# Performance work log

Measured on AMD Instinct MI355X. Metric: run time of the kernel, lower is better.

The kernel has to match this reference:

```python
import jax, jax.numpy as jnp
import numpy as np

CAPACITY = 0.125


def setup_inputs() -> dict:
    key = jax.random.key(0)
    ks = jax.random.split(key, 6)
    b, s, d, dff = 4, 8192, 512, 2048
    x = jax.random.normal(ks[0], (b, s, d), dtype=jnp.float32)
    position_ids = jnp.tile(jnp.arange(s, dtype=jnp.int64)[None, :], (b, 1))
    Wr = jax.random.normal(ks[1], (d,), dtype=jnp.float32) * 0.02
    br = jnp.zeros((1,), dtype=jnp.float32)
    W1 = jax.random.normal(ks[2], (d, dff), dtype=jnp.float32) * 0.02
    b1 = jnp.zeros((dff,), dtype=jnp.float32)
    W2 = jax.random.normal(ks[3], (dff, d), dtype=jnp.float32) * 0.02
    b2 = jnp.zeros((d,), dtype=jnp.float32)
    return {"x": x, "position_ids": position_ids, "Wr": Wr, "br": br,
            "W1": W1, "b1": b1, "W2": W2, "b2": b2}


def reference(x, position_ids, Wr, br, W1, b1, W2, b2):
    b, s, d = x.shape
    # Router: Linear(d, 1) -> squeeze(-1)
    weights = jnp.einsum('bsd,d->bs', x, Wr) + br  # [b, s]
    k = int(CAPACITY * s)
    # Per-batch top-k threshold (k-th largest value)
    top_k_values = jax.lax.top_k(weights, k)[0]  # [b, k], sorted desc
    threshold = top_k_values[:, -1]              # [b]
    selected_mask = weights > threshold[:, None]  # strict >, ties excluded (matches torch)
    # Block: per-token MLP (Linear-GELU-Linear). Per-token ops commute with the
    # gather/scatter, so computing densely and masking is mathematically identical
    # to the original gather -> block -> weighted scatter.
    h = jax.nn.gelu(jnp.einsum('bsd,df->bsf', x, W1) + b1)
    y = jnp.einsum('bsf,fd->bsd', h, W2) + b2
    # processed_tokens (= block_out * router_weight on selected) + x on unselected
    out = jnp.where(selected_mask[..., None], y * weights[..., None], x)
    return out
```

## Files before the change

### kernel.cpp

```cpp
#include <hip/hip_runtime.h>
#include <hip/hip_bf16.h>

#define B_   4
#define S_   8192
#define D_   512
#define DFF_ 2048
#define K_TOP 1024

typedef unsigned short u16;
typedef __attribute__((ext_vector_type(8))) short bf16x8;
typedef __attribute__((ext_vector_type(4))) float floatx4;

__device__ __forceinline__ unsigned f2key(float f){
    unsigned u = __float_as_uint(f);
    return (u & 0x80000000u) ? ~u : (u | 0x80000000u);
}
__device__ __forceinline__ u16 f2b(float f){
    unsigned u = __float_as_uint(f);
    u = (u + 0x7FFFu + ((u >> 16) & 1u)) >> 16;
    return (u16)u;
}
__device__ __forceinline__ float gelu_tanh(float v){
    float c = 0.7978845608028654f * (v + 0.044715f * v * v * v);
    return 0.5f * v * (1.0f + tanhf(c));
}

__global__ __launch_bounds__(256) void wts_copy_kernel(
    const float4* __restrict__ x, float4* __restrict__ out,
    const float4* __restrict__ Wr4, const float* __restrict__ br,
    float* __restrict__ w_all, int* __restrict__ count)
{
    if (blockIdx.x == 0 && threadIdx.x == 0) *count = 0;
    const int wv = threadIdx.x >> 6, lane = threadIdx.x & 63;
    const int token = blockIdx.x * 4 + wv;
    const float4* xt = x + (size_t)token * 128;
    float acc = 0.f;
    #pragma unroll
    for (int i = 0; i < 2; i++){
        int j = lane + i * 64;
        float4 v = xt[j];
        out[(size_t)token * 128 + j] = v;
        float4 wvv = Wr4[j];
        acc += v.x*wvv.x + v.y*wvv.y + v.z*wvv.z + v.w*wvv.w;
    }
    #pragma unroll
    for (int off = 32; off > 0; off >>= 1) acc += __shfl_down(acc, off, 64);
    if (lane == 0) w_all[token] = acc + br[0];
}

__global__ __launch_bounds__(1024) void kth_compact_kernel(
    const float4* __restrict__ w_all4, int* __restrict__ count,
    int* __restrict__ idx)
{
    __shared__ unsigned keys[S_];
    __shared__ unsigned hist[16][256];
    __shared__ unsigned suffix[256];
    __shared__ unsigned sprefix;
    __shared__ int sremk;
    const int b = blockIdx.x, tid = threadIdx.x, wv = tid >> 6;
    const float4* row4 = w_all4 + (size_t)b * (S_ / 4);

    #pragma unroll
    for (int i = 0; i < 2; i++){
        int j = tid + i * 1024;
        float4 v = row4[j];
        keys[4*j+0] = f2key(v.x); keys[4*j+1] = f2key(v.y);
        keys[4*j+2] = f2key(v.z); keys[4*j+3] = f2key(v.w);
    }
    if (tid == 0){ sprefix = 0u; sremk = K_TOP; }
    __syncthreads();

    for (int pass = 3; pass >= 0; pass--){
        for (int i = tid; i < 16 * 256; i += 1024) ((unsigned*)hist)[i] = 0u;
        __syncthreads();
        const unsigned mask_hi = (pass == 3) ? 0u : (0xFFFFFFFFu << ((pass + 1) * 8));
        const unsigned pfx = sprefix;
        const int shift = pass * 8;
        #pragma unroll
        for (int i = 0; i < 8; i++){
            unsigned key = keys[tid + i * 1024];
            if ((key & mask_hi) == pfx)
                atomicAdd(&hist[wv][(key >> shift) & 255u], 1u);
        }
        __syncthreads();
        if (tid < 256){
            unsigned s = 0;
            #pragma unroll
            for (int h = 0; h < 16; h++) s += hist[h][tid];
            suffix[tid] = s;
        }
        __syncthreads();
        for (int off = 1; off < 256; off <<= 1){
            unsigned v = 0;
            if (tid < 256 && tid + off < 256) v = suffix[tid + off];
            __syncthreads();
            if (tid < 256) suffix[tid] += v;
            __syncthreads();
        }
        const int remk = sremk;
        __syncthreads();
        if (tid < 256){
            unsigned snext = (tid == 255) ? 0u : suffix[tid + 1];
            if (suffix[tid] >= (unsigned)remk && snext < (unsigned)remk){
                sprefix = pfx | ((unsigned)tid << shift);
                sremk = remk - (int)snext;
            }
        }
        __syncthreads();
    }

    const unsigned thr = sprefix;
    #pragma unroll
    for (int i = 0; i < 8; i++){
        int li = tid + i * 1024;
        if (keys[li] > thr){
            int p = atomicAdd(count, 1);
            idx[p] = b * S_ + li;
        }
    }
}

__global__ __launch_bounds__(256) void tconv_kernel(
    const float* __restrict__ src, u16* __restrict__ dst, int R, int C)
{
    __shared__ float tile[32][33];
    const int cb = blockIdx.x * 32, rb = blockIdx.y * 32;
    const int tr = threadIdx.x >> 5, tc = threadIdx.x & 31;
    #pragma unroll
    for (int i = 0; i < 4; i++){
        int r = tr + i * 8;
        tile[r][tc] = src[(size_t)(rb + r) * C + cb + tc];
    }
    __syncthreads();
    #pragma unroll
    for (int i = 0; i < 4; i++){
        int a = tr + i * 8;
        dst[(size_t)(cb + a) * R + rb + tc] = f2b(tile[tc][a]);
    }
}

__global__ __launch_bounds__(256) void ffn1_kernel(
    const float* __restrict__ x, const int* __restrict__ idx,
    const int* __restrict__ countp, const u16* __restrict__ W1bT,
    const float* __restrict__ bias1, u16* __restrict__ H)
{
    __shared__ __align__(16) u16 As[64 * 40];
    __shared__ __align__(16) u16 Bs[64 * 40];
    const int tid = threadIdx.x;
    const int cnt = *countp;
    const int mBlk = blockIdx.x, nBlk = blockIdx.y;
    const int w = tid >> 6, lane = tid & 63;
    const int wm = (w >> 1) * 32, wn = (w & 1) * 32;
    const int fr = lane & 15, kq8 = (lane >> 4) * 8;

    const int sr = tid >> 2;
    const int sk = (tid & 3) * 8;
    const int mgs = mBlk * 64 + sr;
    const int arow = (mgs < cnt) ? idx[mgs] : 0;
    const float* aptr = x + (size_t)arow * D_ + sk;
    const u16* bptr = W1bT + (size_t)(nBlk * 64 + sr) * D_ + sk;

    floatx4 acc00 = {0,0,0,0}, acc01 = {0,0,0,0}, acc10 = {0,0,0,0}, acc11 = {0,0,0,0};

    for (int kt = 0; kt < D_; kt += 32){
        float4 v0 = *(const float4*)(aptr + kt);
        float4 v1 = *(const float4*)(aptr + kt + 4);
        bf16x8 av;
        av[0] = (short)f2b(v0.x); av[1] = (short)f2b(v0.y);
        av[2] = (short)f2b(v0.z); av[3] = (short)f2b(v0.w);
        av[4] = (short)f2b(v1.x); av[5] = (short)f2b(v1.y);
        av[6] = (short)f2b(v1.z); av[7] = (short)f2b(v1.w);
        *(bf16x8*)&As[sr * 40 + sk] = av;
        *(bf16x8*)&Bs[sr * 40 + sk] = *(const bf16x8*)(bptr + kt);
        __syncthreads();
        bf16x8 a0  = *(bf16x8*)&As[(wm + fr) * 40 + kq8];
        bf16x8 a1  = *(bf16x8*)&As[(wm + 16 + fr) * 40 + kq8];
        bf16x8 b0  = *(bf16x8*)&Bs[(wn + fr) * 40 + kq8];
        bf16x8 b1v = *(bf16x8*)&Bs[(wn + 16 + fr) * 40 + kq8];
        acc00 = __builtin_amdgcn_mfma_f32_16x16x32_bf16(a0, b0,  acc00, 0, 0, 0);
        acc01 = __builtin_amdgcn_mfma_f32_16x16x32_bf16(a0, b1v, acc01, 0, 0, 0);
        acc10 = __builtin_amdgcn_mfma_f32_16x16x32_bf16(a1, b0,  acc10, 0, 0, 0);
        acc11 = __builtin_amdgcn_mfma_f32_16x16x32_bf16(a1, b1v, acc11, 0, 0, 0);
        __syncthreads();
    }

    const int rbase = (lane >> 4) * 4;
    #pragma unroll
    for (int mi = 0; mi < 2; mi++){
        floatx4 aN0 = mi ? acc10 : acc00;
        floatx4 aN1 = mi ? acc11 : acc01;
        #pragma unroll
        for (int r = 0; r < 4; r++){
            int mg = mBlk * 64 + wm + mi * 16 + rbase + r;
            if (mg < cnt){
                int c0 = nBlk * 64 + wn + fr;
                int c1 = c0 + 16;
                H[(size_t)mg * DFF_ + c0] = f2b(gelu_tanh(aN0[r] + bias1[c0]));
                H[(size_t)mg * DFF_ + c1] = f2b(gelu_tanh(aN1[r] + bias1[c1]));
            }
        }
    }
}

__global__ __launch_bounds__(256) void ffn2_kernel(
    const u16* __restrict__ H, const int* __restrict__ idx,
    const int* __restrict__ countp, const float* __restrict__ w_all,
    const u16* __restrict__ W2bT, const float* __restrict__ bias2,
    float* __restrict__ out)
{
    __shared__ __align__(16) u16 As[64 * 40];
    __shared__ __align__(16) u16 Bs[64 * 40];
    const int tid = threadIdx.x;
    const int cnt = *countp;
    const int mBlk = blockIdx.x, nBlk = blockIdx.y;
    const int w = tid >> 6, lane = tid & 63;
    const int wm = (w >> 1) * 32, wn = (w & 1) * 32;
    const int fr = lane & 15, kq8 = (lane >> 4) * 8;

    const int sr = tid >> 2;
    const int sk = (tid & 3) * 8;
    const u16* aptr = H + (size_t)(mBlk * 64 + sr) * DFF_ + sk;
    const u16* bptr = W2bT + (size_t)(nBlk * 64 + sr) * DFF_ + sk;

    floatx4 acc00 = {0,0,0,0}, acc01 = {0,0,0,0}, acc10 = {0,0,0,0}, acc11 = {0,0,0,0};

    for (int kt = 0; kt < DFF_; kt += 32){
        *(bf16x8*)&As[sr * 40 + sk] = *(const bf16x8*)(aptr + kt);
        *(bf16x8*)&Bs[sr * 40 + sk] = *(const bf16x8*)(bptr + kt);
        __syncthreads();
        bf16x8 a0  = *(bf16x8*)&As[(wm + fr) * 40 + kq8];
        bf16x8 a1  = *(bf16x8*)&As[(wm + 16 + fr) * 40 + kq8];
        bf16x8 b0  = *(bf16x8*)&Bs[(wn + fr) * 40 + kq8];
        bf16x8 b1v = *(bf16x8*)&Bs[(wn + 16 + fr) * 40 + kq8];
        acc00 = __builtin_amdgcn_mfma_f32_16x16x32_bf16(a0, b0,  acc00, 0, 0, 0);
        acc01 = __builtin_amdgcn_mfma_f32_16x16x32_bf16(a0, b1v, acc01, 0, 0, 0);
        acc10 = __builtin_amdgcn_mfma_f32_16x16x32_bf16(a1, b0,  acc10, 0, 0, 0);
        acc11 = __builtin_amdgcn_mfma_f32_16x16x32_bf16(a1, b1v, acc11, 0, 0, 0);
        __syncthreads();
    }

    const int rbase = (lane >> 4) * 4;
    #pragma unroll
    for (int mi = 0; mi < 2; mi++){
        floatx4 aN0 = mi ? acc10 : acc00;
        floatx4 aN1 = mi ? acc11 : acc01;
        #pragma unroll
        for (int r = 0; r < 4; r++){
            int mg = mBlk * 64 + wm + mi * 16 + rbase + r;
            if (mg < cnt){
                int token = idx[mg];
                float wt = w_all[token];
                int c0 = nBlk * 64 + wn + fr;
                int c1 = c0 + 16;
                out[(size_t)token * D_ + c0] = (aN0[r] + bias2[c0]) * wt;
                out[(size_t)token * D_ + c1] = (aN1[r] + bias2[c1]) * wt;
            }
        }
    }
}

extern "C" void kernel_launch(void* const* d_in, const int* in_sizes, int n_in,
                              void* d_out, int out_size, void* d_ws, size_t ws_size,
                              hipStream_t stream)
{
    const float* x  = (const float*)d_in[0];
    const float* Wr = (const float*)d_in[2];
    const float* br = (const float*)d_in[3];
    const float* W1 = (const float*)d_in[4];
    const float* b1 = (const float*)d_in[5];
    const float* W2 = (const float*)d_in[6];
    const float* b2 = (const float*)d_in[7];
    float* out = (float*)d_out;
    char* ws = (char*)d_ws;

    float*    w_all  = (float*)   (ws + 0);
    int*      count  = (int*)     (ws + 131088);
    int*      idx    = (int*)     (ws + 131104);
    u16*      W1bT   = (u16*)     (ws + 262144);
    u16*      W2bT   = (u16*)     (ws + 2359296);
    u16*      H      = (u16*)     (ws + 4456448);

    tconv_kernel<<<dim3(DFF_/32, D_/32), 256, 0, stream>>>(W1, W1bT, D_, DFF_);
    tconv_kernel<<<dim3(D_/32, DFF_/32), 256, 0, stream>>>(W2, W2bT, DFF_, D_);
    wts_copy_kernel<<<(B_*S_)/4, 256, 0, stream>>>(
        (const float4*)x, (float4*)out, (const float4*)Wr, br, w_all, count);
    kth_compact_kernel<<<B_, 1024, 0, stream>>>((const float4*)w_all, count, idx);
    ffn1_kernel<<<dim3(64, DFF_/64), 256, 0, stream>>>(x, idx, count, W1bT, b1, H);
    ffn2_kernel<<<dim3(64, D_/64), 256, 0, stream>>>(H, idx, count, w_all, W2bT, b2, out);
}
```

Baseline: 212.9 us.

## Pre-tile operands into k-slab layout and use 128x128 MFMA tiles with direct LDS loads

Adds a gather kernel that converts the selected token rows to bf16 in a k-slab tiled layout, reworks the weight conversion to emit the same tiled layout, and writes H in that layout too. The two GEMM kernels now use 128x128 block tiles with 4x4 MFMA per wave and global_load_lds for direct global-to-LDS copies. The goal is more reuse per LDS load and fewer issued load instructions. The cost is an extra kernel launch and fewer blocks, which may leave CUs idle for these small GEMMs.

```diff
diff --git a/kernel.cpp b/kernel.cpp
--- a/kernel.cpp
+++ b/kernel.cpp
@@ -6,6 +6,8 @@
 #define D_   512
 #define DFF_ 2048
 #define K_TOP 1024
+#define KS1  16
+#define KS2  64
 
 typedef unsigned short u16;
 typedef __attribute__((ext_vector_type(8))) short bf16x8;
@@ -23,6 +25,11 @@
 __device__ __forceinline__ float gelu_tanh(float v){
     float c = 0.7978845608028654f * (v + 0.044715f * v * v * v);
     return 0.5f * v * (1.0f + tanhf(c));
+}
+__device__ __forceinline__ void gl_lds16(const void* gptr, void* lptr){
+    auto g = (const __attribute__((address_space(1))) unsigned int*)((uintptr_t)gptr);
+    auto l = (__attribute__((address_space(3))) unsigned int*)((uintptr_t)lptr);
+    __builtin_amdgcn_global_load_lds(g, l, 16, 0, 0);
 }
 
 __global__ __launch_bounds__(256) void wts_copy_kernel(
@@ -120,140 +127,175 @@
     }
 }
 
+__global__ __launch_bounds__(256) void gather_kernel(
+    const float* __restrict__ x, const int* __restrict__ idx,
+    const int* __restrict__ countp, u16* __restrict__ XbT)
+{
+    const int mt = blockIdx.x;
+    const int w = threadIdx.x >> 6, lane = threadIdx.x & 63;
+    const int cnt = *countp;
+    const int ks = lane >> 2, c8 = (lane & 3) * 8;
+    for (int rr = 0; rr < 32; rr++){
+        int r = w * 32 + rr;
+        int mg = mt * 128 + r;
+        float4 v0 = {0,0,0,0}, v1 = {0,0,0,0};
+        if (mg < cnt){
+            const float* xp = x + (size_t)idx[mg] * D_ + lane * 8;
+            v0 = *(const float4*)xp; v1 = *(const float4*)(xp + 4);
+        }
+        bf16x8 bv;
+        bv[0]=(short)f2b(v0.x); bv[1]=(short)f2b(v0.y);
+        bv[2]=(short)f2b(v0.z); bv[3]=(short)f2b(v0.w);
+        bv[4]=(short)f2b(v1.x); bv[5]=(short)f2b(v1.y);
+        bv[6]=(short)f2b(v1.z); bv[7]=(short)f2b(v1.w);
+        *(bf16x8*)&XbT[((size_t)(mt * KS1 + ks) * 128 + r) * 32 + c8] = bv;
+    }
+}
+
 __global__ __launch_bounds__(256) void tconv_kernel(
     const float* __restrict__ src, u16* __restrict__ dst, int R, int C)
 {
-    __shared__ float tile[32][33];
-    const int cb = blockIdx.x * 32, rb = blockIdx.y * 32;
-    const int tr = threadIdx.x >> 5, tc = threadIdx.x & 31;
-    #pragma unroll
-    for (int i = 0; i < 4; i++){
-        int r = tr + i * 8;
-        tile[r][tc] = src[(size_t)(rb + r) * C + cb + tc];
+    __shared__ float tile[32][132];
+    const int nt = blockIdx.x, ks = blockIdx.y;
+    const int n0 = nt * 128, k0 = ks * 32;
+    const int tid = threadIdx.x;
+    #pragma unroll
+    for (int i = 0; i < 16; i++){
+        int lin = tid + i * 256;
+        int kk = lin >> 7, nn = lin & 127;
+        tile[kk][nn] = src[(size_t)(k0 + kk) * C + n0 + nn];
     }
     __syncthreads();
-    #pragma unroll
-    for (int i = 0; i < 4; i++){
-        int a = tr + i * 8;
-        dst[(size_t)(cb + a) * R + rb + tc] = f2b(tile[tc][a]);
+    size_t base = ((size_t)(nt * (R / 32) + ks)) * 4096;
+    #pragma unroll
+    for (int i = 0; i < 2; i++){
+        int chunk = tid + i * 256;
+        int r = chunk >> 2, c8 = (chunk & 3) * 8;
+        bf16x8 bv;
+        #pragma unroll
+        for (int e = 0; e < 8; e++) bv[e] = (short)f2b(tile[c8 + e][r]);
+        *(bf16x8*)&dst[base + r * 32 + c8] = bv;
     }
 }
 
 __global__ __launch_bounds__(256) void ffn1_kernel(
-    const float* __restrict__ x, const int* __restrict__ idx,
-    const int* __restrict__ countp, const u16* __restrict__ W1bT,
-    const float* __restrict__ bias1, u16* __restrict__ H)
-{
-    __shared__ __align__(16) u16 As[64 * 40];
-    __shared__ __align__(16) u16 Bs[64 * 40];
+    const u16* __restrict__ XbT, const u16* __restrict__ W1t,
+    const int* __restrict__ countp, const float* __restrict__ bias1,
+    u16* __restrict__ Ht)
+{
+    __shared__ __align__(16) u16 As[128 * 32];
+    __shared__ __align__(16) u16 Bs[128 * 32];
     const int tid = threadIdx.x;
     const int cnt = *countp;
     const int mBlk = blockIdx.x, nBlk = blockIdx.y;
-    const int w = tid >> 6, lane = tid & 63;
-    const int wm = (w >> 1) * 32, wn = (w & 1) * 32;
-    const int fr = lane & 15, kq8 = (lane >> 4) * 8;
-
-    const int sr = tid >> 2;
-    const int sk = (tid & 3) * 8;
-    const int mgs = mBlk * 64 + sr;
-    const int arow = (mgs < cnt) ? idx[mgs] : 0;
-    const float* aptr = x + (size_t)arow * D_ + sk;
-    const u16* bptr = W1bT + (size_t)(nBlk * 64 + sr) * D_ + sk;
-
-    floatx4 acc00 = {0,0,0,0}, acc01 = {0,0,0,0}, acc10 = {0,0,0,0}, acc11 = {0,0,0,0};
-
-    for (int kt = 0; kt < D_; kt += 32){
-        float4 v0 = *(const float4*)(aptr + kt);
-        float4 v1 = *(const float4*)(aptr + kt + 4);
-        bf16x8 av;
-        av[0] = (short)f2b(v0.x); av[1] = (short)f2b(v0.y);
-        av[2] = (short)f2b(v0.z); av[3] = (short)f2b(v0.w);
-        av[4] = (short)f2b(v1.x); av[5] = (short)f2b(v1.y);
-        av[6] = (short)f2b(v1.z); av[7] = (short)f2b(v1.w);
-        *(bf16x8*)&As[sr * 40 + sk] = av;
-        *(bf16x8*)&Bs[sr * 40 + sk] = *(const bf16x8*)(bptr + kt);
-        __syncthreads();
-        bf16x8 a0  = *(bf16x8*)&As[(wm + fr) * 40 + kq8];
-        bf16x8 a1  = *(bf16x8*)&As[(wm + 16 + fr) * 40 + kq8];
-        bf16x8 b0  = *(bf16x8*)&Bs[(wn + fr) * 40 + kq8];
-        bf16x8 b1v = *(bf16x8*)&Bs[(wn + 16 + fr) * 40 + kq8];
-        acc00 = __builtin_amdgcn_mfma_f32_16x16x32_bf16(a0, b0,  acc00, 0, 0, 0);
-        acc01 = __builtin_amdgcn_mfma_f32_16x16x32_bf16(a0, b1v, acc01, 0, 0, 0);
-        acc10 = __builtin_amdgcn_mfma_f32_16x16x32_bf16(a1, b0,  acc10, 0, 0, 0);
-        acc11 = __builtin_amdgcn_mfma_f32_16x16x32_bf16(a1, b1v, acc11, 0, 0, 0);
-        __syncthreads();
-    }
-
-    const int rbase = (lane >> 4) * 4;
-    #pragma unroll
-    for (int mi = 0; mi < 2; mi++){
-        floatx4 aN0 = mi ? acc10 : acc00;
-        floatx4 aN1 = mi ? acc11 : acc01;
-        #pragma unroll
-        for (int r = 0; r < 4; r++){
-            int mg = mBlk * 64 + wm + mi * 16 + rbase + r;
+    const int lane = tid & 63, w = tid >> 6;
+    const int wr = (w >> 1) * 64, wc = (w & 1) * 64;
+    const int fr = lane & 15, quad = lane >> 4, kq8 = quad * 8;
+
+    const char* Ag = (const char*)(XbT + (size_t)mBlk * KS1 * 4096) + tid * 16;
+    const char* Bg = (const char*)(W1t + (size_t)nBlk * KS1 * 4096) + tid * 16;
+    char* Al = (char*)As + tid * 16;
+    char* Bl = (char*)Bs + tid * 16;
+
+    floatx4 acc[4][4] = {};
+    for (int ksi = 0; ksi < KS1; ksi++){
+        gl_lds16(Ag, Al); gl_lds16(Ag + 4096, Al + 4096);
+        gl_lds16(Bg, Bl); gl_lds16(Bg + 4096, Bl + 4096);
+        Ag += 8192; Bg += 8192;
+        __syncthreads();
+        bf16x8 af[4], bf[4];
+        #pragma unroll
+        for (int i = 0; i < 4; i++) af[i] = *(const bf16x8*)&As[(wr + i*16 + fr) * 32 + kq8];
+        #pragma unroll
+        for (int j = 0; j < 4; j++) bf[j] = *(const bf16x8*)&Bs[(wc + j*16 + fr) * 32 + kq8];
+        #pragma unroll
+        for (int i = 0; i < 4; i++)
+            #pragma unroll
+            for (int j = 0; j < 4; j++)
+                acc[i][j] = __builtin_amdgcn_mfma_f32_16x16x32_bf16(af[i], bf[j], acc[i][j], 0, 0, 0);
+        __syncthreads();
+    }
+
+    float bj[4];
+    #pragma unroll
+    for (int j = 0; j < 4; j++) bj[j] = bias1[nBlk*128 + wc + j*16 + fr];
+    const int rbase = quad * 4;
+    #pragma unroll
+    for (int i = 0; i < 4; i++){
+        int r128b = wr + i*16 + rbase;
+        #pragma unroll
+        for (int rg = 0; rg < 4; rg++){
+            int r128 = r128b + rg;
+            int mg = mBlk*128 + r128;
             if (mg < cnt){
-                int c0 = nBlk * 64 + wn + fr;
-                int c1 = c0 + 16;
-                H[(size_t)mg * DFF_ + c0] = f2b(gelu_tanh(aN0[r] + bias1[c0]));
-                H[(size_t)mg * DFF_ + c1] = f2b(gelu_tanh(aN1[r] + bias1[c1]));
+                #pragma unroll
+                for (int j = 0; j < 4; j++){
+                    int n = nBlk*128 + wc + j*16 + fr;
+                    float v = gelu_tanh(acc[i][j][rg] + bj[j]);
+                    Ht[((size_t)(mBlk * KS2 + (n >> 5)) * 128 + r128) * 32 + (n & 31)] = f2b(v);
+                }
             }
         }
     }
 }
 
 __global__ __launch_bounds__(256) void ffn2_kernel(
-    const u16* __restrict__ H, const int* __restrict__ idx,
-    const int* __restrict__ countp, const float* __restrict__ w_all,
-    const u16* __restrict__ W2bT, const float* __restrict__ bias2,
+    const u16* __restrict__ Ht, const u16* __restrict__ W2t,
+    const int* __restrict__ countp, const int* __restrict__ idx,
+    const float* __restrict__ w_all, const float* __restrict__ bias2,
     float* __restrict__ out)
 {
-    __shared__ __align__(16) u16 As[64 * 40];
-    __shared__ __align__(16) u16 Bs[64 * 40];
+    __shared__ __align__(16) u16 As[128 * 32];
+    __shared__ __align__(16) u16 Bs[128 * 32];
     const int tid = threadIdx.x;
     const int cnt = *countp;
     const int mBlk = blockIdx.x, nBlk = blockIdx.y;
-    const int w = tid >> 6, lane = tid & 63;
-    const int wm = (w >> 1) * 32, wn = (w & 1) * 32;
-    const int fr = lane & 15, kq8 = (lane >> 4) * 8;
-
-    const int sr = tid >> 2;
-    const int sk = (tid & 3) * 8;
-    const u16* aptr = H + (size_t)(mBlk * 64 + sr) * DFF_ + sk;
-    const u16* bptr = W2bT + (size_t)(nBlk * 64 + sr) * DFF_ + sk;
-
-    floatx4 acc00 = {0,0,0,0}, acc01 = {0,0,0,0}, acc10 = {0,0,0,0}, acc11 = {0,0,0,0};
-
-    for (int kt = 0; kt < DFF_; kt += 32){
-        *(bf16x8*)&As[sr * 40 + sk] = *(const bf16x8*)(aptr + kt);
-        *(bf16x8*)&Bs[sr * 40 + sk] = *(const bf16x8*)(bptr + kt);
-        __syncthreads();
-        bf16x8 a0  = *(bf16x8*)&As[(wm + fr) * 40 + kq8];
-        bf16x8 a1  = *(bf16x8*)&As[(wm + 16 + fr) * 40 + kq8];
-        bf16x8 b0  = *(bf16x8*)&Bs[(wn + fr) * 40 + kq8];
-        bf16x8 b1v = *(bf16x8*)&Bs[(wn + 16 + fr) * 40 + kq8];
-        acc00 = __builtin_amdgcn_mfma_f32_16x16x32_bf16(a0, b0,  acc00, 0, 0, 0);
-        acc01 = __builtin_amdgcn_mfma_f32_16x16x32_bf16(a0, b1v, acc01, 0, 0, 0);
-        acc10 = __builtin_amdgcn_mfma_f32_16x16x32_bf16(a1, b0,  acc10, 0, 0, 0);
-        acc11 = __builtin_amdgcn_mfma_f32_16x16x32_bf16(a1, b1v, acc11, 0, 0, 0);
-        __syncthreads();
-    }
-
-    const int rbase = (lane >> 4) * 4;
-    #pragma unroll
-    for (int mi = 0; mi < 2; mi++){
-        floatx4 aN0 = mi ? acc10 : acc00;
-        floatx4 aN1 = mi ? acc11 : acc01;
-        #pragma unroll
-        for (int r = 0; r < 4; r++){
-            int mg = mBlk * 64 + wm + mi * 16 + rbase + r;
+    const int lane = tid & 63, w = tid >> 6;
+    const int wr = (w >> 1) * 64, wc = (w & 1) * 64;
+    const int fr = lane & 15, quad = lane >> 4, kq8 = quad * 8;
+
+    const char* Ag = (const char*)(Ht + (size_t)mBlk * KS2 * 4096) + tid * 16;
+    const char* Bg = (const char*)(W2t + (size_t)nBlk * KS2 * 4096) + tid * 16;
+    char* Al = (char*)As + tid * 16;
+    char* Bl = (char*)Bs + tid * 16;
+
+    floatx4 acc[4][4] = {};
+    for (int ksi = 0; ksi < KS2; ksi++){
+        gl_lds16(Ag, Al); gl_lds16(Ag + 4096, Al + 4096);
+        gl_lds16(Bg, Bl); gl_lds16(Bg + 4096, Bl + 4096);
+        Ag += 8192; Bg += 8192;
+        __syncthreads();
+        bf16x8 af[4], bf[4];
+        #pragma unroll
+        for (int i = 0; i < 4; i++) af[i] = *(const bf16x8*)&As[(wr + i*16 + fr) * 32 + kq8];
+        #pragma unroll
+        for (int j = 0; j < 4; j++) bf[j] = *(const bf16x8*)&Bs[(wc + j*16 + fr) * 32 + kq8];
+        #pragma unroll
+        for (int i = 0; i < 4; i++)
+            #pragma unroll
+            for (int j = 0; j < 4; j++)
+                acc[i][j] = __builtin_amdgcn_mfma_f32_16x16x32_bf16(af[i], bf[j], acc[i][j], 0, 0, 0);
+        __syncthreads();
+    }
+
+    float bj[4];
+    #pragma unroll
+    for (int j = 0; j < 4; j++) bj[j] = bias2[nBlk*128 + wc + j*16 + fr];
+    const int rbase = quad * 4;
+    #pragma unroll
+    for (int i = 0; i < 4; i++){
+        #pragma unroll
+        for (int rg = 0; rg < 4; rg++){
+            int mg = mBlk*128 + wr + i*16 + rbase + rg;
             if (mg < cnt){
                 int token = idx[mg];
                 float wt = w_all[token];
-                int c0 = nBlk * 64 + wn + fr;
-                int c1 = c0 + 16;
-                out[(size_t)token * D_ + c0] = (aN0[r] + bias2[c0]) * wt;
-                out[(size_t)token * D_ + c1] = (aN1[r] + bias2[c1]) * wt;
+                float* op = out + (size_t)token * D_;
+                #pragma unroll
+                for (int j = 0; j < 4; j++){
+                    int n = nBlk*128 + wc + j*16 + fr;
+                    op[n] = (acc[i][j][rg] + bj[j]) * wt;
+                }
             }
         }
     }
@@ -273,18 +315,20 @@
     float* out = (float*)d_out;
     char* ws = (char*)d_ws;
 
-    float*    w_all  = (float*)   (ws + 0);
-    int*      count  = (int*)     (ws + 131088);
-    int*      idx    = (int*)     (ws + 131104);
-    u16*      W1bT   = (u16*)     (ws + 262144);
-    u16*      W2bT   = (u16*)     (ws + 2359296);
-    u16*      H      = (u16*)     (ws + 4456448);
-
-    tconv_kernel<<<dim3(DFF_/32, D_/32), 256, 0, stream>>>(W1, W1bT, D_, DFF_);
-    tconv_kernel<<<dim3(D_/32, DFF_/32), 256, 0, stream>>>(W2, W2bT, DFF_, D_);
+    float* w_all = (float*)(ws + 0);
+    int*   count = (int*)  (ws + 131088);
+    int*   idx   = (int*)  (ws + 131104);
+    u16*   XbT   = (u16*)  (ws + 262144);
+    u16*   W1t   = (u16*)  (ws + 4456448);
+    u16*   W2t   = (u16*)  (ws + 6553600);
+    u16*   Ht    = (u16*)  (ws + 8650752);
+
+    tconv_kernel<<<dim3(DFF_/128, D_/32),  256, 0, stream>>>(W1, W1t, D_, DFF_);
+    tconv_kernel<<<dim3(D_/128,  DFF_/32), 256, 0, stream>>>(W2, W2t, DFF_, D_);
     wts_copy_kernel<<<(B_*S_)/4, 256, 0, stream>>>(
         (const float4*)x, (float4*)out, (const float4*)Wr, br, w_all, count);
     kth_compact_kernel<<<B_, 1024, 0, stream>>>((const float4*)w_all, count, idx);
-    ffn1_kernel<<<dim3(64, DFF_/64), 256, 0, stream>>>(x, idx, count, W1bT, b1, H);
-    ffn2_kernel<<<dim3(64, D_/64), 256, 0, stream>>>(H, idx, count, w_all, W2bT, b2, out);
-}
+    gather_kernel<<<32, 256, 0, stream>>>(x, idx, count, XbT);
+    ffn1_kernel<<<dim3(32, DFF_/128), 256, 0, stream>>>(XbT, W1t, count, b1, Ht);
+    ffn2_kernel<<<dim3(32, D_/128),   256, 0, stream>>>(Ht, W2t, count, idx, w_all, b2, out);
+}
```

Measured after the change: 246.5 us. 1.16x slower.
